# Kernel optimization log

Hardware: AMD Instinct MI355X
Metric: run time of the kernel (lower is better)

## Reference

```python
import jax, jax.numpy as jnp
import numpy as np

N_NODES = 20000
N_EDGES = 320000
DIM_IN = 768
DIM_H = 512
S_HOPS = 3
NUM_GNNS = 4
NEG_SLOPE = 0.2  # DGL GATConv default


def setup_inputs() -> dict:
    key = jax.random.key(0)
    ks = jax.random.split(key, 12)
    feat = jax.random.normal(ks[0], (N_NODES, DIM_IN), dtype=jnp.float32)
    src = jax.random.randint(ks[1], (N_EDGES,), 0, N_NODES)
    dst = jax.random.randint(ks[2], (N_EDGES,), 0, N_NODES)
    # learned params
    fc_W = jax.random.normal(ks[3], (DIM_IN, DIM_H), dtype=jnp.float32) * 0.02
    fc_b = jnp.zeros((DIM_H,), dtype=jnp.float32)
    gat_W = jax.random.normal(ks[4], (NUM_GNNS, DIM_H, DIM_H), dtype=jnp.float32) * 0.02
    gat_al = jax.random.normal(ks[5], (NUM_GNNS, DIM_H), dtype=jnp.float32) * 0.1
    gat_ar = jax.random.normal(ks[6], (NUM_GNNS, DIM_H), dtype=jnp.float32) * 0.1
    gat_b = jnp.zeros((NUM_GNNS, DIM_H), dtype=jnp.float32)
    beta = jnp.ones((S_HOPS + 1,), dtype=jnp.float32)
    return {"feat": feat, "fc_W": fc_W, "fc_b": fc_b, "gat_W": gat_W,
            "gat_al": gat_al, "gat_ar": gat_ar, "gat_b": gat_b,
            "beta": beta, "src": src, "dst": dst}


def _gat_layer(h, W, a_l, a_r, b, src, dst):
    z = h @ W                                   # [N, DH]
    el = z @ a_l                                # [N]
    er = z @ a_r                                # [N]
    e = jax.nn.leaky_relu(el[src] + er[dst], NEG_SLOPE)  # [E]
    # edge softmax over incoming edges of each dst node
    m = jax.ops.segment_max(e, dst, num_segments=N_NODES)
    ex = jnp.exp(e - m[dst])
    denom = jax.ops.segment_sum(ex, dst, num_segments=N_NODES)
    alpha = ex / denom[dst]                     # [E]
    out = jax.ops.segment_sum(alpha[:, None] * z[src], dst, num_segments=N_NODES)
    return out + b


def reference(feat, fc_W, fc_b, gat_W, gat_al, gat_ar, gat_b, beta, src, dst):
    h = feat @ fc_W + fc_b                      # dim_in -> 512
    for l in range(NUM_GNNS):
        h = _gat_layer(h, gat_W[l], gat_al[l], gat_ar[l], gat_b[l], src, dst)
    # A_hat = A + I propagation; A_hat @ Z = scatter(Z[src] -> dst) + Z
    Z_prev = h
    Z = beta[0] * Z_prev                        # accumulated Z is computed but the
    for s in range(1, S_HOPS + 1):              # original module returns Z_prev
        Z_s = jax.ops.segment_sum(Z_prev[src], dst, num_segments=N_NODES) + Z_prev
        Z = Z + beta[s] * Z_s
        Z_prev = Z_s
    return Z_prev
```

## Files before the change

### kernel.cpp

```cpp
#include <hip/hip_runtime.h>
#include <math.h>

#define N_NODES 20000
#define M_PAD   20096
#define N_EDGES 320000
#define DIM_IN 768
#define DIM_H 512
#define NUM_GNNS 4
#define NEG_SLOPE 0.2f

#define GEMM_TILES 628
#define GEMM_GRID  632

#define SLC_GRID 5000

typedef __attribute__((ext_vector_type(8))) short short8;
typedef __attribute__((ext_vector_type(4))) float f32x4;

#define GPTR(p) (const __attribute__((address_space(1))) void*)(p)
#define LPTR(p) (__attribute__((address_space(3))) void*)(p)

__device__ __forceinline__ float bf2f(unsigned int lo16) {
  return __uint_as_float(lo16 << 16);
}
__device__ __forceinline__ unsigned short f2bf(float f) {
  unsigned int u = __float_as_uint(f);
  u += 0x7FFFu + ((u >> 16) & 1u);
  return (unsigned short)(u >> 16);
}
__device__ __forceinline__ void unpack8(uint4 v, float* f) {
  f[0] = bf2f(v.x & 0xffffu); f[1] = bf2f(v.x >> 16);
  f[2] = bf2f(v.y & 0xffffu); f[3] = bf2f(v.y >> 16);
  f[4] = bf2f(v.z & 0xffffu); f[5] = bf2f(v.z >> 16);
  f[6] = bf2f(v.w & 0xffffu); f[7] = bf2f(v.w >> 16);
}
__device__ __forceinline__ uint4 pack8(const float* o) {
  uint4 pv;
  pv.x = (unsigned)f2bf(o[0]) | ((unsigned)f2bf(o[1]) << 16);
  pv.y = (unsigned)f2bf(o[2]) | ((unsigned)f2bf(o[3]) << 16);
  pv.z = (unsigned)f2bf(o[4]) | ((unsigned)f2bf(o[5]) << 16);
  pv.w = (unsigned)f2bf(o[6]) | ((unsigned)f2bf(o[7]) << 16);
  return pv;
}

__device__ __forceinline__ float waveReduceSum(float v) {
#pragma unroll
  for (int off = 32; off > 0; off >>= 1) v += __shfl_xor(v, off, 64);
  return v;
}
__device__ __forceinline__ float waveReduceMax(float v) {
#pragma unroll
  for (int off = 32; off > 0; off >>= 1) v = fmaxf(v, __shfl_xor(v, off, 64));
  return v;
}

__global__ __launch_bounds__(256) void gemm_mfma_bf16(
    const unsigned short* __restrict__ A,
    const unsigned short* __restrict__ Bt,
    const float* __restrict__ bias,
    unsigned short* __restrict__ Cbf,
    int K) {
  int bid = blockIdx.x;
  int tile = (bid & 7) * (GEMM_GRID / 8) + (bid >> 3);
  if (tile >= GEMM_TILES) return;
  int brow = tile >> 2;
  int bcol = tile & 3;

  __shared__ __align__(16) unsigned short lds[4][128 * 32];
  int tid = threadIdx.x;
  int wave = tid >> 6, lane = tid & 63;
  int wm = wave >> 1, wn = wave & 1;

  int rl = lane >> 2;
  int kc = (lane & 3) ^ ((lane >> 3) & 3);
  int r0 = 32 * wave;
  const unsigned short* gA0 = A + (size_t)(brow * 128 + r0 + rl) * K + kc * 8;
  const unsigned short* gA1 = gA0 + (size_t)16 * K;
  const unsigned short* gB0 = Bt + (size_t)(bcol * 128 + r0 + rl) * K + kc * 8;
  const unsigned short* gB1 = gB0 + (size_t)16 * K;

  int mrow = lane & 15;
  int q = lane >> 4;
  int swz = (q ^ ((mrow >> 1) & 3)) * 8;

  f32x4 acc[4][4];
#pragma unroll
  for (int i = 0; i < 4; ++i)
#pragma unroll
    for (int j = 0; j < 4; ++j) acc[i][j] = (f32x4)(0.f);

  int nk = K >> 5;
  {
    unsigned short* lA = lds[0] + r0 * 32;
    unsigned short* lB = lds[2] + r0 * 32;
    __builtin_amdgcn_global_load_lds(GPTR(gA0), LPTR(lA), 16, 0, 0);
    __builtin_amdgcn_global_load_lds(GPTR(gA1), LPTR(lA + 512), 16, 0, 0);
    __builtin_amdgcn_global_load_lds(GPTR(gB0), LPTR(lB), 16, 0, 0);
    __builtin_amdgcn_global_load_lds(GPTR(gB1), LPTR(lB + 512), 16, 0, 0);
  }
  __syncthreads();

  for (int t = 0; t < nk; ++t) {
    int cur = t & 1;
    if (t + 1 < nk) {
      int k0 = (t + 1) << 5;
      unsigned short* lA = lds[cur ^ 1] + r0 * 32;
      unsigned short* lB = lds[2 + (cur ^ 1)] + r0 * 32;
      __builtin_amdgcn_global_load_lds(GPTR(gA0 + k0), LPTR(lA), 16, 0, 0);
      __builtin_amdgcn_global_load_lds(GPTR(gA1 + k0), LPTR(lA + 512), 16, 0, 0);
      __builtin_amdgcn_global_load_lds(GPTR(gB0 + k0), LPTR(lB), 16, 0, 0);
      __builtin_amdgcn_global_load_lds(GPTR(gB1 + k0), LPTR(lB + 512), 16, 0, 0);
    }
    const short8* ra = (const short8*)(lds[cur] + (64 * wm + mrow) * 32 + swz);
    const short8* rb = (const short8*)(lds[2 + cur] + (64 * wn + mrow) * 32 + swz);
    short8 a[4], b[4];
#pragma unroll
    for (int u = 0; u < 4; ++u) a[u] = ra[u * 64];
#pragma unroll
    for (int u = 0; u < 4; ++u) b[u] = rb[u * 64];
#pragma unroll
    for (int mt = 0; mt < 4; ++mt)
#pragma unroll
      for (int nt = 0; nt < 4; ++nt)
        acc[mt][nt] = __builtin_amdgcn_mfma_f32_16x16x32_bf16(a[mt], b[nt], acc[mt][nt], 0, 0, 0);
    __syncthreads();
  }

  unsigned short* Cs = lds[0];
  {
    float bv[4];
#pragma unroll
    for (int nt = 0; nt < 4; ++nt)
      bv[nt] = bias ? bias[bcol * 128 + 64 * wn + 16 * nt + mrow] : 0.f;
#pragma unroll
    for (int mt = 0; mt < 4; ++mt)
#pragma unroll
      for (int nt = 0; nt < 4; ++nt)
#pragma unroll
        for (int i = 0; i < 4; ++i) {
          int row = 64 * wm + 16 * mt + 4 * q + i;
          int col = 64 * wn + 16 * nt + mrow;
          Cs[row * 128 + col] = f2bf(acc[mt][nt][i] + bv[nt]);
        }
  }
  __syncthreads();
  int rr = tid >> 4, cb = (tid & 15) * 8;
#pragma unroll
  for (int it = 0; it < 8; ++it, rr += 16) {
    uint4 val = *(const uint4*)(Cs + rr * 128 + cb);
    *(uint4*)(Cbf + (size_t)(brow * 128 + rr) * DIM_H + bcol * 128 + cb) = val;
  }
}

__global__ void convert_feat(const float* __restrict__ feat, unsigned short* __restrict__ Abf) {
  int t = blockIdx.x * blockDim.x + threadIdx.x;
  const int CHUNKS = M_PAD * DIM_IN / 8;
  if (t >= CHUNKS) return;
  int row = t / (DIM_IN / 8);
  uint4 o;
  if (row < N_NODES) {
    const float4* p = (const float4*)(feat + (size_t)t * 8);
    float4 x = p[0], y = p[1];
    o.x = (unsigned)f2bf(x.x) | ((unsigned)f2bf(x.y) << 16);
    o.y = (unsigned)f2bf(x.z) | ((unsigned)f2bf(x.w) << 16);
    o.z = (unsigned)f2bf(y.x) | ((unsigned)f2bf(y.y) << 16);
    o.w = (unsigned)f2bf(y.z) | ((unsigned)f2bf(y.w) << 16);
  } else {
    o = make_uint4(0, 0, 0, 0);
  }
  ((uint4*)Abf)[t] = o;
}

__global__ __launch_bounds__(256) void transpose_bf16(const float* __restrict__ in,
                                                      unsigned short* __restrict__ out,
                                                      int R, int C) {
  __shared__ float tile[32][33];
  int tx = threadIdx.x, ty = threadIdx.y;
  size_t base = (size_t)blockIdx.z * R * C;
  int r0 = blockIdx.x * 32, c0 = blockIdx.y * 32;
#pragma unroll
  for (int i = 0; i < 4; ++i) {
    int r = r0 + ty + i * 8;
    tile[ty + i * 8][tx] = in[base + (size_t)r * C + c0 + tx];
  }
  __syncthreads();
#pragma unroll
  for (int i = 0; i < 4; ++i) {
    int c = c0 + ty + i * 8;
    out[base + (size_t)c * R + r0 + tx] = f2bf(tile[tx][ty + i * 8]);
  }
}

__global__ void count_edges(const int* __restrict__ dst, int* __restrict__ counts) {
  int k = blockIdx.x * blockDim.x + threadIdx.x;
  if (k < N_EDGES) atomicAdd(&counts[dst[k]], 1);
}

__global__ __launch_bounds__(1024) void scan_kernel(const int* __restrict__ counts,
                                                    int* __restrict__ indptr) {
  __shared__ int part[1024];
  int tid = threadIdx.x;
  const int CH = (N_NODES + 1023) / 1024;
  int base = tid * CH;
  int s = 0;
  for (int i = 0; i < CH; ++i) {
    int idx = base + i;
    if (idx < N_NODES) s += counts[idx];
  }
  part[tid] = s;
  __syncthreads();
  for (int off = 1; off < 1024; off <<= 1) {
    int v = (tid >= off) ? part[tid - off] : 0;
    __syncthreads();
    part[tid] += v;
    __syncthreads();
  }
  int run = (tid == 0) ? 0 : part[tid - 1];
  for (int i = 0; i < CH; ++i) {
    int idx = base + i;
    if (idx < N_NODES) {
      indptr[idx] = run;
      run += counts[idx];
      if (idx == N_NODES - 1) indptr[N_NODES] = run;
    }
  }
}

__global__ void fill_adj(const int* __restrict__ src, const int* __restrict__ dst,
                         const int* __restrict__ indptr, int* __restrict__ cursor,
                         int* __restrict__ adjsrc) {
  int k = blockIdx.x * blockDim.x + threadIdx.x;
  if (k < N_EDGES) {
    int d = dst[k];
    int pos = atomicAdd(&cursor[d], 1);
    adjsrc[indptr[d] + pos] = src[k];
  }
}

__global__ void pack_ones(const int* __restrict__ adjsrc, int2* __restrict__ apairs) {
  int k = blockIdx.x * blockDim.x + threadIdx.x;
  if (k < N_EDGES) apairs[k] = make_int2(adjsrc[k], __float_as_int(1.0f));
}

__global__ __launch_bounds__(256) void eler_bf(const unsigned short* __restrict__ zbf,
                                               const float* __restrict__ al,
                                               const float* __restrict__ ar,
                                               float* __restrict__ el, float* __restrict__ er) {
  int wid = (blockIdx.x * blockDim.x + threadIdx.x) >> 6;
  int lane = threadIdx.x & 63;
  if (wid >= N_NODES) return;
  uint4 zv = ((const uint4*)(zbf + (size_t)wid * DIM_H))[lane];
  float z[8];
  unpack8(zv, z);
  const float4* al4 = (const float4*)(al + lane * 8);
  const float4* ar4 = (const float4*)(ar + lane * 8);
  float4 a0 = al4[0], a1 = al4[1], r0 = ar4[0], r1 = ar4[1];
  float sl = z[0] * a0.x + z[1] * a0.y + z[2] * a0.z + z[3] * a0.w +
             z[4] * a1.x + z[5] * a1.y + z[6] * a1.z + z[7] * a1.w;
  float sr = z[0] * r0.x + z[1] * r0.y + z[2] * r0.z + z[3] * r0.w +
             z[4] * r1.x + z[5] * r1.y + z[6] * r1.z + z[7] * r1.w;
  sl = waveReduceSum(sl);
  sr = waveReduceSum(sr);
  if (lane == 0) { el[wid] = sl; er[wid] = sr; }
}

__global__ __launch_bounds__(256) void edge_softmax_alpha(
    const float* __restrict__ el, const float* __restrict__ er,
    const int* __restrict__ indptr, const int* __restrict__ adjsrc,
    float* __restrict__ alpha, int2* __restrict__ apairs) {
  int v = (blockIdx.x * blockDim.x + threadIdx.x) >> 6;
  int lane = threadIdx.x & 63;
  if (v >= N_NODES) return;
  int begin = indptr[v], end = indptr[v + 1];
  float er_v = er[v];

  float m = -INFINITY;
  for (int j = begin + lane; j < end; j += 64) {
    float e = el[adjsrc[j]] + er_v;
    e = (e >= 0.f) ? e : NEG_SLOPE * e;
    alpha[j] = e;
    m = fmaxf(m, e);
  }
  m = waveReduceMax(m);

  float ss = 0.f;
  for (int j = begin + lane; j < end; j += 64) {
    float ex = __expf(alpha[j] - m);
    alpha[j] = ex;
    ss += ex;
  }
  float denom = waveReduceSum(ss);
  float inv = (end > begin) ? 1.f / denom : 0.f;

  for (int j = begin + lane; j < end; j += 64)
    apairs[j] = make_int2(adjsrc[j], __float_as_int(alpha[j] * inv));
}

__global__ __launch_bounds__(256) void gather_slc(
    const unsigned short* __restrict__ zin, const int2* __restrict__ apairs,
    const int* __restrict__ indptr, const float* __restrict__ bias, int self_term,
    unsigned short* __restrict__ out_bf, float* __restrict__ out_f32) {
  int slice = blockIdx.x & 7;
  int grp = blockIdx.x >> 3;
  int wave = threadIdx.x >> 6, lane = threadIdx.x & 63;
  int slot = lane >> 3, sub = lane & 7;
  int v = grp * 32 + wave * 8 + slot;
  unsigned cbyte = (unsigned)(slice * 128 + sub * 16);
  const char* zb = (const char*)zin;
  const char* pb = (const char*)apairs;

  int b = indptr[v];
  int deg = indptr[v + 1] - b;
  int md = deg;
  md = max(md, __shfl_xor(md, 8, 64));
  md = max(md, __shfl_xor(md, 16, 64));
  md = max(md, __shfl_xor(md, 32, 64));

  float acc[8];
  if (self_term) {
    uint4 sz = *(const uint4*)(zb + (((unsigned)v) << 10) + cbyte);
    unpack8(sz, acc);
  } else {
#pragma unroll
    for (int i = 0; i < 8; ++i) acc[i] = 0.f;
  }

  const unsigned NMAX = (unsigned)(N_NODES - 1);
  unsigned ab = ((unsigned)b) << 3;
  int2 ra[8];
#pragma unroll
  for (int u = 0; u < 8; ++u) ra[u] = *(const int2*)(pb + ab + u * 8);
#pragma nounroll
  for (int t = 0; t < md; t += 8) {
    int2 rn[8];
    if (t + 8 < md) {
#pragma unroll
      for (int u = 0; u < 8; ++u) rn[u] = *(const int2*)(pb + ab + 64 + u * 8);
    } else {
#pragma unroll
      for (int u = 0; u < 8; ++u) rn[u] = ra[u];
    }
    int rem = deg - t;
#pragma unroll
    for (int u = 0; u < 8; ++u) {
      unsigned uidx = min((unsigned)ra[u].x, NMAX);
      float wv = (u < rem) ? __int_as_float(ra[u].y) : 0.f;
      uint4 z = *(const uint4*)(zb + (uidx << 10) + cbyte);
      float f[8];
      unpack8(z, f);
#pragma unroll
      for (int i = 0; i < 8; ++i) acc[i] = fmaf(wv, f[i], acc[i]);
    }
#pragma unroll
    for (int u = 0; u < 8; ++u) ra[u] = rn[u];
    ab += 64;
  }

  if (bias) {
    const float4* b4 = (const float4*)(bias + slice * 64 + sub * 8);
    float4 b0 = b4[0], b1 = b4[1];
    acc[0] += b0.x; acc[1] += b0.y; acc[2] += b0.z; acc[3] += b0.w;
    acc[4] += b1.x; acc[5] += b1.y; acc[6] += b1.z; acc[7] += b1.w;
  }
  if (out_bf) {
    uint4 pv = pack8(acc);
    *(uint4*)((char*)out_bf + (((unsigned)v) << 10) + cbyte) = pv;
  } else {
    char* p = (char*)out_f32 + (((unsigned)v) << 11) + cbyte * 2;
    *(f32x4*)p = (f32x4){acc[0], acc[1], acc[2], acc[3]};
    *(f32x4*)(p + 16) = (f32x4){acc[4], acc[5], acc[6], acc[7]};
  }
}

extern "C" void kernel_launch(void* const* d_in, const int* in_sizes, int n_in,
                              void* d_out, int out_size, void* d_ws, size_t ws_size,
                              hipStream_t stream) {
  const float* feat = (const float*)d_in[0];
  const float* fc_W = (const float*)d_in[1];
  const float* fc_b = (const float*)d_in[2];
  const float* gat_W = (const float*)d_in[3];
  const float* gat_al = (const float*)d_in[4];
  const float* gat_ar = (const float*)d_in[5];
  const float* gat_b = (const float*)d_in[6];
  const int* src = (const int*)d_in[8];
  const int* dst = (const int*)d_in[9];
  float* out = (float*)d_out;

  char* w = (char*)d_ws;
  auto alloc = [&](size_t bytes) {
    char* p = w;
    w += (bytes + 255) & ~(size_t)255;
    return p;
  };
  unsigned short* hbf   = (unsigned short*)alloc((size_t)M_PAD * DIM_H * 2);
  unsigned short* fcWt  = (unsigned short*)alloc((size_t)DIM_H * DIM_IN * 2);
  unsigned short* gatWt = (unsigned short*)alloc((size_t)NUM_GNNS * DIM_H * DIM_H * 2);
  float* el    = (float*)alloc((size_t)N_NODES * 4);
  float* er    = (float*)alloc((size_t)N_NODES * 4);
  int* counts  = (int*)alloc((size_t)2 * N_NODES * 4);
  int* cursor  = counts + N_NODES;
  int* indptr  = (int*)alloc((size_t)(N_NODES + 1) * 4);
  int* adjsrc  = (int*)alloc((size_t)(N_EDGES + 64) * 4);
  char* uni = alloc((size_t)M_PAD * DIM_IN * 2);
  unsigned short* Abf = (unsigned short*)uni;
  float* alpha = (float*)uni;
  unsigned short* Z1  = (unsigned short*)uni;
  int2* apairs = (int2*)(uni + (size_t)M_PAD * DIM_H * 2);
  unsigned short* zbf = (unsigned short*)d_out;

  hipMemsetAsync(counts, 0, sizeof(int) * 2 * N_NODES, stream);
  count_edges<<<(N_EDGES + 255) / 256, 256, 0, stream>>>(dst, counts);
  scan_kernel<<<1, 1024, 0, stream>>>(counts, indptr);
  fill_adj<<<(N_EDGES + 255) / 256, 256, 0, stream>>>(src, dst, indptr, cursor, adjsrc);

  convert_feat<<<(M_PAD * DIM_IN / 8 + 255) / 256, 256, 0, stream>>>(feat, Abf);
  transpose_bf16<<<dim3(DIM_IN / 32, DIM_H / 32, 1), dim3(32, 8), 0, stream>>>(fc_W, fcWt, DIM_IN, DIM_H);
  transpose_bf16<<<dim3(DIM_H / 32, DIM_H / 32, NUM_GNNS), dim3(32, 8), 0, stream>>>(gat_W, gatWt, DIM_H, DIM_H);

  gemm_mfma_bf16<<<GEMM_GRID, 256, 0, stream>>>(Abf, fcWt, fc_b, hbf, DIM_IN);

  int nwaveblocks = (N_NODES * 64 + 255) / 256;
  for (int l = 0; l < NUM_GNNS; ++l) {
    gemm_mfma_bf16<<<GEMM_GRID, 256, 0, stream>>>(hbf, gatWt + (size_t)l * DIM_H * DIM_H,
                                                  nullptr, zbf, DIM_H);
    eler_bf<<<nwaveblocks, 256, 0, stream>>>(zbf, gat_al + (size_t)l * DIM_H,
                                             gat_ar + (size_t)l * DIM_H, el, er);
    edge_softmax_alpha<<<nwaveblocks, 256, 0, stream>>>(el, er, indptr, adjsrc, alpha, apairs);
    gather_slc<<<SLC_GRID, 256, 0, stream>>>(
        zbf, apairs, indptr, gat_b + (size_t)l * DIM_H, 0, hbf, nullptr);
  }

  pack_ones<<<(N_EDGES + 255) / 256, 256, 0, stream>>>(adjsrc, apairs);
  gather_slc<<<SLC_GRID, 256, 0, stream>>>(hbf, apairs, indptr, nullptr, 1, Z1, nullptr);
  gather_slc<<<SLC_GRID, 256, 0, stream>>>(Z1, apairs, indptr, nullptr, 1, hbf, nullptr);
  gather_slc<<<SLC_GRID, 256, 0, stream>>>(hbf, apairs, indptr, nullptr, 1, nullptr, out);
}
```

Measured before the change: 581.7 us.

## Fuse attention logits into GEMM epilogue and degree-sort nodes for gather

Removes the separate el/er kernel: each GEMM tile computes partial dot products of its output tile with a_l/a_r from LDS and atomically adds them into zeroed el/er buffers, which requires a memset per layer. It also adds a per-256-node window permutation that groups nodes by in-degree bucket, so the 8 nodes sharing a wave in the gather kernel have similar degrees and less divergence. The gather kernel switches to 128-thread blocks with twice the grid. Costs are float atomics and nondeterministic summation order in el/er, plus an extra indirection through perm.

```diff
diff --git a/kernel.cpp b/kernel.cpp
--- a/kernel.cpp
+++ b/kernel.cpp
@@ -12,7 +12,7 @@
 #define GEMM_TILES 628
 #define GEMM_GRID  632
 
-#define SLC_GRID 5000
+#define SLC_GRID 10000
 
 typedef __attribute__((ext_vector_type(8))) short short8;
 typedef __attribute__((ext_vector_type(4))) float f32x4;
@@ -59,7 +59,9 @@
     const unsigned short* __restrict__ Bt,
     const float* __restrict__ bias,
     unsigned short* __restrict__ Cbf,
-    int K) {
+    int K,
+    const float* __restrict__ al, const float* __restrict__ ar,
+    float* __restrict__ el, float* __restrict__ er) {
   int bid = blockIdx.x;
   int tile = (bid & 7) * (GEMM_GRID / 8) + (bid >> 3);
   if (tile >= GEMM_TILES) return;
@@ -126,7 +128,7 @@
     __syncthreads();
   }
 
-  unsigned short* Cs = lds[0];
+  unsigned short* Cs = &lds[0][0];
   {
     float bv[4];
 #pragma unroll
@@ -149,6 +151,34 @@
   for (int it = 0; it < 8; ++it, rr += 16) {
     uint4 val = *(const uint4*)(Cs + rr * 128 + cb);
     *(uint4*)(Cbf + (size_t)(brow * 128 + rr) * DIM_H + bcol * 128 + cb) = val;
+  }
+
+  if (al) {
+    int r2 = tid >> 1;
+    int ch = (tid & 1) * 64;
+    const float* alp = al + bcol * 128 + ch;
+    const float* arp = ar + bcol * 128 + ch;
+    float sl = 0.f, sr = 0.f;
+#pragma unroll
+    for (int c8 = 0; c8 < 64; c8 += 8) {
+      uint4 zz = *(const uint4*)(Cs + r2 * 128 + ch + c8);
+      float zf[8];
+      unpack8(zz, zf);
+      const float4* a4 = (const float4*)(alp + c8);
+      const float4* r4 = (const float4*)(arp + c8);
+      float4 a0 = a4[0], a1 = a4[1], b0 = r4[0], b1 = r4[1];
+      sl += zf[0]*a0.x + zf[1]*a0.y + zf[2]*a0.z + zf[3]*a0.w +
+            zf[4]*a1.x + zf[5]*a1.y + zf[6]*a1.z + zf[7]*a1.w;
+      sr += zf[0]*b0.x + zf[1]*b0.y + zf[2]*b0.z + zf[3]*b0.w +
+            zf[4]*b1.x + zf[5]*b1.y + zf[6]*b1.z + zf[7]*b1.w;
+    }
+    sl += __shfl_xor(sl, 1, 64);
+    sr += __shfl_xor(sr, 1, 64);
+    if ((tid & 1) == 0) {
+      int row = brow * 128 + r2;
+      atomicAdd(&el[row], sl);
+      atomicAdd(&er[row], sr);
+    }
   }
 }
 
@@ -237,31 +267,36 @@
   }
 }
 
+__global__ __launch_bounds__(256) void build_perm_win(const int* __restrict__ counts,
+                                                      int* __restrict__ perm) {
+  __shared__ int hist[64];
+  __shared__ int basec[64];
+  int tid = threadIdx.x;
+  int v0 = blockIdx.x * 256;
+  int n = min(256, N_NODES - v0);
+  if (tid < 64) hist[tid] = 0;
+  __syncthreads();
+  int b = 0;
+  if (tid < n) {
+    b = min(counts[v0 + tid], 63);
+    atomicAdd(&hist[b], 1);
+  }
+  __syncthreads();
+  if (tid == 0) {
+    int run = 0;
+#pragma unroll
+    for (int i = 0; i < 64; ++i) { basec[i] = run; run += hist[i]; }
+  }
+  __syncthreads();
+  if (tid < n) {
+    int pos = atomicAdd(&basec[b], 1);
+    perm[v0 + pos] = v0 + tid;
+  }
+}
+
 __global__ void pack_ones(const int* __restrict__ adjsrc, int2* __restrict__ apairs) {
   int k = blockIdx.x * blockDim.x + threadIdx.x;
   if (k < N_EDGES) apairs[k] = make_int2(adjsrc[k], __float_as_int(1.0f));
-}
-
-__global__ __launch_bounds__(256) void eler_bf(const unsigned short* __restrict__ zbf,
-                                               const float* __restrict__ al,
-                                               const float* __restrict__ ar,
-                                               float* __restrict__ el, float* __restrict__ er) {
-  int wid = (blockIdx.x * blockDim.x + threadIdx.x) >> 6;
-  int lane = threadIdx.x & 63;
-  if (wid >= N_NODES) return;
-  uint4 zv = ((const uint4*)(zbf + (size_t)wid * DIM_H))[lane];
-  float z[8];
-  unpack8(zv, z);
-  const float4* al4 = (const float4*)(al + lane * 8);
-  const float4* ar4 = (const float4*)(ar + lane * 8);
-  float4 a0 = al4[0], a1 = al4[1], r0 = ar4[0], r1 = ar4[1];
-  float sl = z[0] * a0.x + z[1] * a0.y + z[2] * a0.z + z[3] * a0.w +
-             z[4] * a1.x + z[5] * a1.y + z[6] * a1.z + z[7] * a1.w;
-  float sr = z[0] * r0.x + z[1] * r0.y + z[2] * r0.z + z[3] * r0.w +
-             z[4] * r1.x + z[5] * r1.y + z[6] * r1.z + z[7] * r1.w;
-  sl = waveReduceSum(sl);
-  sr = waveReduceSum(sr);
-  if (lane == 0) { el[wid] = sl; er[wid] = sr; }
 }
 
 __global__ __launch_bounds__(256) void edge_softmax_alpha(
@@ -296,15 +331,17 @@
     apairs[j] = make_int2(adjsrc[j], __float_as_int(alpha[j] * inv));
 }
 
-__global__ __launch_bounds__(256) void gather_slc(
+__global__ __launch_bounds__(128) void gather_slc(
     const unsigned short* __restrict__ zin, const int2* __restrict__ apairs,
-    const int* __restrict__ indptr, const float* __restrict__ bias, int self_term,
+    const int* __restrict__ indptr, const int* __restrict__ perm,
+    const float* __restrict__ bias, int self_term,
     unsigned short* __restrict__ out_bf, float* __restrict__ out_f32) {
   int slice = blockIdx.x & 7;
   int grp = blockIdx.x >> 3;
   int wave = threadIdx.x >> 6, lane = threadIdx.x & 63;
   int slot = lane >> 3, sub = lane & 7;
-  int v = grp * 32 + wave * 8 + slot;
+  int vidx = grp * 16 + wave * 8 + slot;
+  int v = perm[vidx];
   unsigned cbyte = (unsigned)(slice * 128 + sub * 16);
   const char* zb = (const char*)zin;
   const char* pb = (const char*)apairs;
@@ -395,12 +432,13 @@
   unsigned short* hbf   = (unsigned short*)alloc((size_t)M_PAD * DIM_H * 2);
   unsigned short* fcWt  = (unsigned short*)alloc((size_t)DIM_H * DIM_IN * 2);
   unsigned short* gatWt = (unsigned short*)alloc((size_t)NUM_GNNS * DIM_H * DIM_H * 2);
-  float* el    = (float*)alloc((size_t)N_NODES * 4);
-  float* er    = (float*)alloc((size_t)N_NODES * 4);
+  float* el    = (float*)alloc((size_t)2 * M_PAD * 4);
+  float* er    = el + M_PAD;
   int* counts  = (int*)alloc((size_t)2 * N_NODES * 4);
   int* cursor  = counts + N_NODES;
   int* indptr  = (int*)alloc((size_t)(N_NODES + 1) * 4);
   int* adjsrc  = (int*)alloc((size_t)(N_EDGES + 64) * 4);
+  int* perm    = (int*)alloc((size_t)N_NODES * 4);
   char* uni = alloc((size_t)M_PAD * DIM_IN * 2);
   unsigned short* Abf = (unsigned short*)uni;
   float* alpha = (float*)uni;
@@ -412,26 +450,28 @@
   count_edges<<<(N_EDGES + 255) / 256, 256, 0, stream>>>(dst, counts);
   scan_kernel<<<1, 1024, 0, stream>>>(counts, indptr);
   fill_adj<<<(N_EDGES + 255) / 256, 256, 0, stream>>>(src, dst, indptr, cursor, adjsrc);
+  build_perm_win<<<(N_NODES + 255) / 256, 256, 0, stream>>>(counts, perm);
 
   convert_feat<<<(M_PAD * DIM_IN / 8 + 255) / 256, 256, 0, stream>>>(feat, Abf);
   transpose_bf16<<<dim3(DIM_IN / 32, DIM_H / 32, 1), dim3(32, 8), 0, stream>>>(fc_W, fcWt, DIM_IN, DIM_H);
   transpose_bf16<<<dim3(DIM_H / 32, DIM_H / 32, NUM_GNNS), dim3(32, 8), 0, stream>>>(gat_W, gatWt, DIM_H, DIM_H);
 
-  gemm_mfma_bf16<<<GEMM_GRID, 256, 0, stream>>>(Abf, fcWt, fc_b, hbf, DIM_IN);
+  gemm_mfma_bf16<<<GEMM_GRID, 256, 0, stream>>>(Abf, fcWt, fc_b, hbf, DIM_IN,
+                                                nullptr, nullptr, nullptr, nullptr);
 
   int nwaveblocks = (N_NODES * 64 + 255) / 256;
   for (int l = 0; l < NUM_GNNS; ++l) {
-    gemm_mfma_bf16<<<GEMM_GRID, 256, 0, stream>>>(hbf, gatWt + (size_t)l * DIM_H * DIM_H,
-                                                  nullptr, zbf, DIM_H);
-    eler_bf<<<nwaveblocks, 256, 0, stream>>>(zbf, gat_al + (size_t)l * DIM_H,
-                                             gat_ar + (size_t)l * DIM_H, el, er);
+    hipMemsetAsync(el, 0, sizeof(float) * 2 * M_PAD, stream);
+    gemm_mfma_bf16<<<GEMM_GRID, 256, 0, stream>>>(
+        hbf, gatWt + (size_t)l * DIM_H * DIM_H, nullptr, zbf, DIM_H,
+        gat_al + (size_t)l * DIM_H, gat_ar + (size_t)l * DIM_H, el, er);
     edge_softmax_alpha<<<nwaveblocks, 256, 0, stream>>>(el, er, indptr, adjsrc, alpha, apairs);
-    gather_slc<<<SLC_GRID, 256, 0, stream>>>(
-        zbf, apairs, indptr, gat_b + (size_t)l * DIM_H, 0, hbf, nullptr);
+    gather_slc<<<SLC_GRID, 128, 0, stream>>>(
+        zbf, apairs, indptr, perm, gat_b + (size_t)l * DIM_H, 0, hbf, nullptr);
   }
 
   pack_ones<<<(N_EDGES + 255) / 256, 256, 0, stream>>>(adjsrc, apairs);
-  gather_slc<<<SLC_GRID, 256, 0, stream>>>(hbf, apairs, indptr, nullptr, 1, Z1, nullptr);
-  gather_slc<<<SLC_GRID, 256, 0, stream>>>(Z1, apairs, indptr, nullptr, 1, hbf, nullptr);
-  gather_slc<<<SLC_GRID, 256, 0, stream>>>(hbf, apairs, indptr, nullptr, 1, nullptr, out);
-}
+  gather_slc<<<SLC_GRID, 128, 0, stream>>>(hbf, apairs, indptr, perm, nullptr, 1, Z1, nullptr);
+  gather_slc<<<SLC_GRID, 128, 0, stream>>>(Z1, apairs, indptr, perm, nullptr, 1, hbf, nullptr);
+  gather_slc<<<SLC_GRID, 128, 0, stream>>>(hbf, apairs, indptr, perm, nullptr, 1, nullptr, out);
+}
```

Measured after the change: 600.3 us. +3.2%, slower.
